# Kernel tuning notes

Measured on AMD Instinct MI355X. Metric: run time of the kernel, lower is better.

The kernel has to match this reference:

```python
import jax, jax.numpy as jnp
import numpy as np

B, C, P = 32, 192, 3136
EPS = 0.01


def setup_inputs() -> dict:
    key = jax.random.key(0)
    k1, k2, k3 = jax.random.split(key, 3)
    return {
        "embeddings": jax.random.normal(k1, (B, C, P), dtype=jnp.float32),
        "means": jax.random.normal(k2, (P, C), dtype=jnp.float32),
        "covariances": jax.random.normal(k3, (P, C, C), dtype=jnp.float32),
        "n": 96,
    }


def reference(embeddings, means, covariances, n):
    # embeddings: [B, C, P]; means: [P, C] (running sums); covariances: [P, C, C] (running outer-product sums)
    b = embeddings.shape[0]
    c = embeddings.shape[1]
    # Training-branch accumulation: per-patch sum of outer products over the batch,
    # expressed as one batched GEMM instead of P*B tiny torch.outer calls.
    new_means = means + jnp.einsum("bcp->pc", embeddings)
    new_covs = covariances + jnp.einsum("bcp,bdp->pcd", embeddings, embeddings)
    n_new = n + b
    # calculate_means_and_covariances(): finalize sample mean / covariance per patch.
    learned_means = new_means / n_new  # [P, C]
    learned_covs = (new_covs - n_new * jnp.einsum("pc,pd->pcd", learned_means, learned_means)) / (n_new - 1)
    learned_covs = learned_covs + EPS * jnp.eye(c, dtype=learned_covs.dtype)
    return (learned_means, learned_covs)
```

## Files before the change

kernel.cpp:

```cpp
#include <hip/hip_runtime.h>


#define BB 32
#define CC 192
#define PP 3136
#define EPSV 0.01f

__global__ __launch_bounds__(256) void padim_kernel(
    const float* __restrict__ emb,
    const float* __restrict__ means,
    const float* __restrict__ covs,
    const int*   __restrict__ n_ptr,
    float* __restrict__ out_means,
    float* __restrict__ out_covs)
{
    __shared__ __align__(16) float E[BB][CC + 4];
    __shared__ __align__(16) float m[CC];

    const int bid = blockIdx.x;
    const int p = (bid & 7) * (PP / 8) + (bid >> 3);

    const int t = threadIdx.x;

    const float n_new = (float)(n_ptr[0] + BB);
    const float inv_nnew = 1.0f / n_new;
    const float inv_nm1 = 1.0f / (n_new - 1.0f);

    #pragma unroll
    for (int i = t; i < BB * CC; i += 256) {
        const int b = i / CC;
        const int c = i - b * CC;
        E[b][c] = emb[(size_t)i * PP + p];
    }
    __syncthreads();

    if (t < CC) {
        float s = 0.0f;
        #pragma unroll
        for (int b = 0; b < BB; ++b) s += E[b][t];
        const float mm = (means[(size_t)p * CC + t] + s) * inv_nnew;
        m[t] = mm;
        out_means[(size_t)p * CC + t] = mm;
    }
    __syncthreads();

    const int tx = t & 15;
    const int ty = t >> 4;
    const float* __restrict__ cov_p = covs + (size_t)p * CC * CC;
    float* __restrict__ out_p = out_covs + (size_t)p * CC * CC;

    #pragma unroll 1
    for (int pass = 0; pass < 9; ++pass) {
        const int tc = pass / 3;
        const int td = pass - tc * 3;
        const int c0 = tc * 64 + ty * 4;
        const int d0 = td * 64 + tx * 4;

        float acc[4][4] = {{0.f,0.f,0.f,0.f},{0.f,0.f,0.f,0.f},
                           {0.f,0.f,0.f,0.f},{0.f,0.f,0.f,0.f}};

        #pragma unroll 8
        for (int b = 0; b < BB; ++b) {
            const float4 cv = *reinterpret_cast<const float4*>(&E[b][c0]);
            const float4 dv = *reinterpret_cast<const float4*>(&E[b][d0]);
            const float cs[4] = {cv.x, cv.y, cv.z, cv.w};
            const float ds[4] = {dv.x, dv.y, dv.z, dv.w};
            #pragma unroll
            for (int i = 0; i < 4; ++i)
                #pragma unroll
                for (int j = 0; j < 4; ++j)
                    acc[i][j] = fmaf(cs[i], ds[j], acc[i][j]);
        }

        const float4 mc4 = *reinterpret_cast<const float4*>(&m[c0]);
        const float4 md4 = *reinterpret_cast<const float4*>(&m[d0]);
        const float mcs[4] = {mc4.x, mc4.y, mc4.z, mc4.w};
        const float mds[4] = {md4.x, md4.y, md4.z, md4.w};

        #pragma unroll
        for (int i = 0; i < 4; ++i) {
            const int c = c0 + i;
            const size_t row = (size_t)c * CC + d0;
            const float4 cin = *reinterpret_cast<const float4*>(&cov_p[row]);
            const float nm_c = n_new * mcs[i];
            float4 o;
            o.x = (cin.x + acc[i][0] - nm_c * mds[0]) * inv_nm1;
            o.y = (cin.y + acc[i][1] - nm_c * mds[1]) * inv_nm1;
            o.z = (cin.z + acc[i][2] - nm_c * mds[2]) * inv_nm1;
            o.w = (cin.w + acc[i][3] - nm_c * mds[3]) * inv_nm1;
            if (c == d0 + 0) o.x += EPSV;
            if (c == d0 + 1) o.y += EPSV;
            if (c == d0 + 2) o.z += EPSV;
            if (c == d0 + 3) o.w += EPSV;
            *reinterpret_cast<float4*>(&out_p[row]) = o;
        }
    }
}

extern "C" void kernel_launch(void* const* d_in, const int* in_sizes, int n_in,
                              void* d_out, int out_size, void* d_ws, size_t ws_size,
                              hipStream_t stream) {
    const float* emb   = (const float*)d_in[0];
    const float* means = (const float*)d_in[1];
    const float* covs  = (const float*)d_in[2];
    const int*   n_ptr = (const int*)d_in[3];

    float* out_means = (float*)d_out;
    float* out_covs  = (float*)d_out + (size_t)PP * CC;

    hipLaunchKernelGGL(padim_kernel, dim3(PP), dim3(256), 0, stream,
                       emb, means, covs, n_ptr, out_means, out_covs);
}
```

Baseline: 254.3 us.

## Rewrite covariance kernel with bf16 MFMA, two patches per block, prefetch ring

Converts embeddings to bf16 in LDS and computes each per-patch outer-product sum with 16x16x32 bf16 MFMA instructions instead of scalar FP32 FMAs. Each block now handles two patches, which lets the embedding gather use float2 loads. A three-deep register ring prefetches the input covariance rows with nontemporal loads while MFMA results are staged through LDS for coalesced epilogue writes. The bf16 rounding of the embeddings (and of the sums used for the means) reduces precision compared with the FP32 reference, so tolerance could be exceeded.

```diff
diff --git a/kernel.cpp b/kernel.cpp
--- a/kernel.cpp
+++ b/kernel.cpp
@@ -5,8 +5,21 @@
 #define CC 192
 #define PP 3136
 #define EPSV 0.01f
+#define WROW 52
 
-__global__ __launch_bounds__(256) void padim_kernel(
+typedef float f32x4 __attribute__((ext_vector_type(4)));
+typedef short bf16x8 __attribute__((ext_vector_type(8)));
+
+__device__ __forceinline__ unsigned short f2bf(float f) {
+    unsigned int u = __float_as_uint(f);
+    u += 0x7fffu + ((u >> 16) & 1u);
+    return (unsigned short)(u >> 16);
+}
+__device__ __forceinline__ float bf16val(unsigned short u) {
+    return __uint_as_float(((unsigned int)u) << 16);
+}
+
+__global__ __launch_bounds__(256, 3) void padim_fused(
     const float* __restrict__ emb,
     const float* __restrict__ means,
     const float* __restrict__ covs,
@@ -14,85 +27,119 @@
     float* __restrict__ out_means,
     float* __restrict__ out_covs)
 {
-    __shared__ __align__(16) float E[BB][CC + 4];
-    __shared__ __align__(16) float m[CC];
+    __shared__ unsigned short eb[2][CC][40];
+    __shared__ __align__(16) float m_lds[2][CC];
+    __shared__ __align__(16) float wbuf[4][16 * WROW];
 
     const int bid = blockIdx.x;
-    const int p = (bid & 7) * (PP / 8) + (bid >> 3);
+    const int sw = (bid & 7) * (PP / 2 / 8) + (bid >> 3);
+    const int p0 = sw * 2;
 
     const int t = threadIdx.x;
+    const int lane = t & 63;
+    const int w = t >> 6;
+    const int l15 = lane & 15;
+    const int l4  = lane >> 4;
 
     const float n_new = (float)(n_ptr[0] + BB);
     const float inv_nnew = 1.0f / n_new;
     const float inv_nm1 = 1.0f / (n_new - 1.0f);
 
-    #pragma unroll
-    for (int i = t; i < BB * CC; i += 256) {
+    #pragma unroll 8
+    for (int k = 0; k < 24; ++k) {
+        const int i = k * 256 + t;
         const int b = i / CC;
         const int c = i - b * CC;
-        E[b][c] = emb[(size_t)i * PP + p];
+        const float2 v = *reinterpret_cast<const float2*>(&emb[(size_t)i * PP + p0]);
+        eb[0][c][b] = f2bf(v.x);
+        eb[1][c][b] = f2bf(v.y);
     }
     __syncthreads();
 
-    if (t < CC) {
-        float s = 0.0f;
+    for (int r = t; r < 2 * CC; r += 256) {
+        const int j = r / CC;
+        const int c = r - j * CC;
+        float s = 0.f;
         #pragma unroll
-        for (int b = 0; b < BB; ++b) s += E[b][t];
-        const float mm = (means[(size_t)p * CC + t] + s) * inv_nnew;
-        m[t] = mm;
-        out_means[(size_t)p * CC + t] = mm;
+        for (int q = 0; q < 16; ++q) {
+            const unsigned int u = *reinterpret_cast<const unsigned int*>(&eb[j][c][2 * q]);
+            s += bf16val((unsigned short)(u & 0xffffu)) + bf16val((unsigned short)(u >> 16));
+        }
+        const size_t idx = (size_t)(p0 + j) * CC + c;
+        const float mm = (means[idx] + s) * inv_nnew;
+        m_lds[j][c] = mm;
+        out_means[idx] = mm;
     }
     __syncthreads();
 
-    const int tx = t & 15;
-    const int ty = t >> 4;
-    const float* __restrict__ cov_p = covs + (size_t)p * CC * CC;
-    float* __restrict__ out_p = out_covs + (size_t)p * CC * CC;
+    int rk[3], qk[3], offb[3];
+    #pragma unroll
+    for (int k = 0; k < 3; ++k) {
+        const int chunk = k * 64 + lane;
+        rk[k] = chunk / 12;
+        qk[k] = chunk - rk[k] * 12;
+        offb[k] = rk[k] * CC + 48 * w + 4 * qk[k];
+    }
 
     #pragma unroll 1
-    for (int pass = 0; pass < 9; ++pass) {
-        const int tc = pass / 3;
-        const int td = pass - tc * 3;
-        const int c0 = tc * 64 + ty * 4;
-        const int d0 = td * 64 + tx * 4;
+    for (int j = 0; j < 2; ++j) {
+        const float* __restrict__ cov_p = covs + (size_t)(p0 + j) * CC * CC;
+        float* __restrict__ out_p = out_covs + (size_t)(p0 + j) * CC * CC;
+        const float* __restrict__ mj = &m_lds[j][0];
 
-        float acc[4][4] = {{0.f,0.f,0.f,0.f},{0.f,0.f,0.f,0.f},
-                           {0.f,0.f,0.f,0.f},{0.f,0.f,0.f,0.f}};
+        bf16x8 Af[3];
+        #pragma unroll
+        for (int dt = 0; dt < 3; ++dt)
+            Af[dt] = *reinterpret_cast<const bf16x8*>(&eb[j][(3 * w + dt) * 16 + l15][l4 * 8]);
 
-        #pragma unroll 8
-        for (int b = 0; b < BB; ++b) {
-            const float4 cv = *reinterpret_cast<const float4*>(&E[b][c0]);
-            const float4 dv = *reinterpret_cast<const float4*>(&E[b][d0]);
-            const float cs[4] = {cv.x, cv.y, cv.z, cv.w};
-            const float ds[4] = {dv.x, dv.y, dv.z, dv.w};
+        f32x4 mdk[3];
+        #pragma unroll
+        for (int k = 0; k < 3; ++k)
+            mdk[k] = *reinterpret_cast<const f32x4*>(&mj[48 * w + 4 * qk[k]]);
+
+        f32x4 cin[3][3];
+        #pragma unroll
+        for (int pt = 0; pt < 2; ++pt)
             #pragma unroll
-            for (int i = 0; i < 4; ++i)
-                #pragma unroll
-                for (int j = 0; j < 4; ++j)
-                    acc[i][j] = fmaf(cs[i], ds[j], acc[i][j]);
-        }
-
-        const float4 mc4 = *reinterpret_cast<const float4*>(&m[c0]);
-        const float4 md4 = *reinterpret_cast<const float4*>(&m[d0]);
-        const float mcs[4] = {mc4.x, mc4.y, mc4.z, mc4.w};
-        const float mds[4] = {md4.x, md4.y, md4.z, md4.w};
+            for (int k = 0; k < 3; ++k)
+                cin[pt][k] = __builtin_nontemporal_load(reinterpret_cast<const f32x4*>(
+                    cov_p + (size_t)(pt * 16) * CC + offb[k]));
 
         #pragma unroll
-        for (int i = 0; i < 4; ++i) {
-            const int c = c0 + i;
-            const size_t row = (size_t)c * CC + d0;
-            const float4 cin = *reinterpret_cast<const float4*>(&cov_p[row]);
-            const float nm_c = n_new * mcs[i];
-            float4 o;
-            o.x = (cin.x + acc[i][0] - nm_c * mds[0]) * inv_nm1;
-            o.y = (cin.y + acc[i][1] - nm_c * mds[1]) * inv_nm1;
-            o.z = (cin.z + acc[i][2] - nm_c * mds[2]) * inv_nm1;
-            o.w = (cin.w + acc[i][3] - nm_c * mds[3]) * inv_nm1;
-            if (c == d0 + 0) o.x += EPSV;
-            if (c == d0 + 1) o.y += EPSV;
-            if (c == d0 + 2) o.z += EPSV;
-            if (c == d0 + 3) o.w += EPSV;
-            *reinterpret_cast<float4*>(&out_p[row]) = o;
+        for (int ct = 0; ct < 12; ++ct) {
+            if (ct < 10) {
+                const int ring2 = (ct + 2) % 3;
+                #pragma unroll
+                for (int k = 0; k < 3; ++k)
+                    cin[ring2][k] = __builtin_nontemporal_load(reinterpret_cast<const f32x4*>(
+                        cov_p + (size_t)((ct + 2) * 16) * CC + offb[k]));
+            }
+            const bf16x8 Bf = *reinterpret_cast<const bf16x8*>(&eb[j][ct * 16 + l15][l4 * 8]);
+            f32x4 a[3];
+            #pragma unroll
+            for (int dt = 0; dt < 3; ++dt)
+                a[dt] = __builtin_amdgcn_mfma_f32_16x16x32_bf16(
+                    Af[dt], Bf, (f32x4){0.f, 0.f, 0.f, 0.f}, 0, 0, 0);
+
+            #pragma unroll
+            for (int dt = 0; dt < 3; ++dt)
+                *reinterpret_cast<f32x4*>(&wbuf[w][l15 * WROW + (dt * 4 + l4) * 4]) = a[dt];
+
+            const int cbase = ct * 16;
+            const int ring = ct % 3;
+            #pragma unroll
+            for (int k = 0; k < 3; ++k) {
+                const f32x4 av = *reinterpret_cast<const f32x4*>(&wbuf[w][rk[k] * WROW + 4 * qk[k]]);
+                const int c = cbase + rk[k];
+                const float nmc = n_new * mj[c];
+                f32x4 o = (cin[ring][k] + av - nmc * mdk[k]) * inv_nm1;
+                const int dd = c - (48 * w + 4 * qk[k]);
+                o.x += (dd == 0) ? EPSV : 0.f;
+                o.y += (dd == 1) ? EPSV : 0.f;
+                o.z += (dd == 2) ? EPSV : 0.f;
+                o.w += (dd == 3) ? EPSV : 0.f;
+                *reinterpret_cast<f32x4*>(out_p + (size_t)cbase * CC + offb[k]) = o;
+            }
         }
     }
 }
@@ -108,6 +155,6 @@
     float* out_means = (float*)d_out;
     float* out_covs  = (float*)d_out + (size_t)PP * CC;
 
-    hipLaunchKernelGGL(padim_kernel, dim3(PP), dim3(256), 0, stream,
+    hipLaunchKernelGGL(padim_fused, dim3(PP / 2), dim3(256), 0, stream,
                        emb, means, covs, n_ptr, out_means, out_covs);
 }
```

Result: slower. 338.0 us (+32.9%).
